# Optimization experiments

Hardware: AMD Instinct MI355X
Metric: run time of the kernel (lower is better)

## Reference

```python
import jax, jax.numpy as jnp
import numpy as np

N_NODES = 50000
N_EDGES = 800000
NDIM_IN = 64
EDIMS = 64
NDIM_OUT = 128


def setup_inputs() -> dict:
    key = jax.random.key(0)
    k = jax.random.split(key, 8)
    nfeats = jax.random.normal(k[0], (N_NODES, NDIM_IN), dtype=jnp.float32)
    efeats = jax.random.normal(k[1], (N_EDGES, EDIMS), dtype=jnp.float32)
    # Linear weights stored as [in, out]; scaled for stable activations.
    W_msg = jax.random.normal(k[2], (NDIM_IN + EDIMS, NDIM_OUT), dtype=jnp.float32) * 0.05
    b_msg = jax.random.normal(k[3], (NDIM_OUT,), dtype=jnp.float32) * 0.05
    W_apply = jax.random.normal(k[4], (NDIM_IN + NDIM_OUT, NDIM_OUT), dtype=jnp.float32) * 0.05
    b_apply = jax.random.normal(k[5], (NDIM_OUT,), dtype=jnp.float32) * 0.05
    src = jax.random.randint(k[6], (N_EDGES,), 0, N_NODES, dtype=jnp.int64)
    dst = jax.random.randint(k[7], (N_EDGES,), 0, N_NODES, dtype=jnp.int64)
    return {
        "nfeats": nfeats,
        "efeats": efeats,
        "W_msg": W_msg,
        "b_msg": b_msg,
        "W_apply": W_apply,
        "b_apply": b_apply,
        "src": src,
        "dst": dst,
    }


def reference(nfeats, efeats, W_msg, b_msg, W_apply, b_apply, src, dst):
    # message: per-edge gather src node feats, concat with edge feats, linear+relu
    msg_in = jnp.concatenate([nfeats[src], efeats], axis=1)          # [E, ndim_in+edims]
    m = jax.nn.relu(msg_in @ W_msg + b_msg)                           # [E, ndim_out]
    # aggregate: sum messages into destination nodes
    h_neigh = jax.ops.segment_sum(m, dst, num_segments=nfeats.shape[0])  # [N, ndim_out]
    # update: concat original node feats with aggregated messages, linear+relu
    out = jax.nn.relu(jnp.concatenate([nfeats, h_neigh], axis=1) @ W_apply + b_apply)
    return out
```

## Files before the change

### kernel.cpp

```cpp
#include <hip/hip_runtime.h>
#include <hip/hip_bf16.h>

#define N_NODES  50000
#define N_EDGES  800000
#define NDIM_IN  64
#define EDIMS    64
#define NDIM_OUT 128

typedef __bf16 bf16;
typedef bf16  bf16x8 __attribute__((ext_vector_type(8)));
typedef float f32x4  __attribute__((ext_vector_type(4)));

__device__ __forceinline__ bool detect_f32(const void* nfeats) {
    const unsigned short* w = (const unsigned short*)nfeats;
    for (int i = 0; i < 64; i += 2) {
        const int e = (w[i] >> 7) & 0xFF;
        if (e < 100 || e > 134) return true;
    }
    return false;
}
__device__ __forceinline__ bool detect_i64(const int* p) {
    for (int i = 1; i < 64; i += 2) if (p[i] != 0) return false;
    return true;
}

__device__ __forceinline__ bf16x8 load8(const void* p, long off, bool f32) {
    if (f32) {
        const float* q = (const float*)p + off;
        const f32x4 a = *(const f32x4*)q;
        const f32x4 b = *(const f32x4*)(q + 4);
        bf16x8 r;
        #pragma unroll
        for (int u = 0; u < 4; ++u) { r[u] = (bf16)a[u]; r[4 + u] = (bf16)b[u]; }
        return r;
    }
    return *(const bf16x8*)((const bf16*)p + off);
}
__device__ __forceinline__ float loadf(const void* p, long i, bool f32) {
    return f32 ? ((const float*)p)[i] : (float)((const bf16*)p)[i];
}
__device__ __forceinline__ void storef(void* p, long i, float v, bool f32) {
    if (f32) ((float*)p)[i] = v; else ((bf16*)p)[i] = (bf16)v;
}

__global__ __launch_bounds__(256) void nf2bf_kernel(const void* __restrict__ nfeats,
                                                    bf16* __restrict__ tbl) {
    __shared__ int s_flags;
    if (threadIdx.x == 0) s_flags = detect_f32(nfeats) ? 1 : 0;
    __syncthreads();
    const bool f32 = (s_flags & 1) != 0;
    const int total  = N_NODES * 64 / 8;
    const int stride = gridDim.x * blockDim.x;
    for (int i = blockIdx.x * blockDim.x + threadIdx.x; i < total; i += stride)
        *(bf16x8*)(tbl + (size_t)i * 8) = load8(nfeats, (long)i * 8, f32);
}

__global__ __launch_bounds__(256) void hist_kernel(const int* __restrict__ dst,
                                                   int* __restrict__ cnt) {
    __shared__ int s_ish;
    if (threadIdx.x == 0) s_ish = detect_i64(dst) ? 1 : 0;
    __syncthreads();
    const int ish = s_ish;
    const int stride = gridDim.x * blockDim.x;
    for (int e = blockIdx.x * blockDim.x + threadIdx.x; e < N_EDGES; e += stride)
        atomicAdd(&cnt[dst[(long)e << ish]], 1);
}

__global__ __launch_bounds__(1024) void scan_kernel(int* __restrict__ cnt,
                                                    int* __restrict__ row_ptr) {
    __shared__ int sw[16];
    const int t    = threadIdx.x;
    const int lane = t & 63;
    const int w    = t >> 6;
    const int base = t * 52;

    int sum = 0;
    #pragma unroll
    for (int j = 0; j < 13; ++j) {
        const int4 q = *(const int4*)(cnt + base + j * 4);
        sum += q.x + q.y + q.z + q.w;
    }
    int s = sum;
    #pragma unroll
    for (int off = 1; off < 64; off <<= 1) {
        const int u = __shfl_up(s, off, 64);
        if (lane >= off) s += u;
    }
    if (lane == 63) sw[w] = s;
    __syncthreads();
    if (t < 16) {
        int x = sw[t];
        #pragma unroll
        for (int off = 1; off < 16; off <<= 1) {
            const int u = __shfl_up(x, off, 16);
            if ((t & 15) >= off) x += u;
        }
        sw[t] = x;
    }
    __syncthreads();
    int run = (w > 0 ? sw[w - 1] : 0) + (s - sum);
    #pragma unroll
    for (int j = 0; j < 13; ++j) {
        const int4 q = *(const int4*)(cnt + base + j * 4);
        int4 r;
        r.x = run; run += q.x;
        r.y = run; run += q.y;
        r.z = run; run += q.z;
        r.w = run; run += q.w;
        *(int4*)(row_ptr + base + j * 4) = r;
        *(int4*)(cnt     + base + j * 4) = r;
    }
}

__global__ __launch_bounds__(256) void gather_kernel(
    const void* __restrict__ nfsrc,
    const void* __restrict__ efeats,
    const int*  __restrict__ src,
    const int*  __restrict__ dst,
    int*        __restrict__ cursor,
    bf16*       __restrict__ A,
    const int   tbl)
{
    __shared__ int s_flags;
    const int tid = threadIdx.x;
    if (tid == 0)
        s_flags = (detect_f32(efeats) ? 1 : 0) | (detect_i64(dst) ? 2 : 0);
    __syncthreads();
    const bool f32 = (s_flags & 1) != 0;
    const int  ish = (s_flags & 2) ? 1 : 0;

    const int lane = tid & 63;
    const int wave = tid >> 6;
    const int q    = lane & 15;
    const int ei   = lane >> 4;

    const int ngroups = N_EDGES / 4;
    const int nw      = gridDim.x * 4;
    for (int g = blockIdx.x * 4 + wave; g < ngroups; g += nw) {
        const int e = g * 4 + ei;
        int pos = 0;
        if (q == 0) pos = atomicAdd(&cursor[dst[(long)e << ish]], 1);
        pos = __shfl(pos, lane & 48, 64);

        bf16x8 v;
        if (q < 8) {
            const int s_ = src[(long)e << ish];
            v = tbl ? *(const bf16x8*)((const bf16*)nfsrc + (size_t)s_ * 64 + q * 8)
                    : load8(nfsrc, (long)s_ * 64 + q * 8, f32);
        } else {
            v = load8(efeats, (long)e * 64 + (q - 8) * 8, f32);
        }
        *(bf16x8*)(A + (size_t)pos * 128 + q * 8) = v;
    }
}

__global__ __launch_bounds__(256) void msg_agg_dense(
    const void* __restrict__ nfeats,
    const bf16* __restrict__ A,
    const void* __restrict__ W_msg,
    const void* __restrict__ b_msg,
    const int*  __restrict__ row_ptr,
    float*      __restrict__ h_neigh)
{
    __shared__ bf16 sWT[128 * 136];
    __shared__ int s_flags;

    const int tid = threadIdx.x;
    if (tid == 0) s_flags = detect_f32(nfeats) ? 1 : 0;
    __syncthreads();
    const bool f32 = (s_flags & 1) != 0;

    #pragma unroll
    for (int it = 0; it < 8; ++it) {
        const int task = it * 256 + tid;
        const int n    = task & 127;
        const int kb8  = task >> 7;
        bf16x8 w;
        #pragma unroll
        for (int j = 0; j < 8; ++j)
            w[j] = (bf16)loadf(W_msg, (long)(kb8 * 8 + j) * 128 + n, f32);
        *(bf16x8*)(sWT + n * 136 + kb8 * 8) = w;
    }
    __syncthreads();

    const int wave = tid >> 6;
    const int lane = tid & 63;
    const int m    = lane & 15;
    const int quad = lane >> 4;

    float bias[8];
    #pragma unroll
    for (int t = 0; t < 8; ++t) bias[t] = loadf(b_msg, t * 16 + m, f32);

    const int wstride = gridDim.x * 4;
    for (int v = blockIdx.x * 4 + wave; v < N_NODES; v += wstride) {
        const int beg = row_ptr[v];
        const int deg = row_ptr[v + 1] - beg;

        float hacc[8] = {0.f, 0.f, 0.f, 0.f, 0.f, 0.f, 0.f, 0.f};

        for (int T = 0; T * 16 < deg; ++T) {
            const int r0 = T * 16;
            const int sl = (r0 + m < deg) ? (beg + r0 + m) : beg;
            const bf16* ap = A + (size_t)sl * 128 + quad * 8;

            bf16x8 a[4];
            #pragma unroll
            for (int kb = 0; kb < 4; ++kb)
                a[kb] = *(const bf16x8*)(ap + kb * 32);

            #pragma unroll
            for (int t = 0; t < 8; ++t) {
                f32x4 acc = {0.f, 0.f, 0.f, 0.f};
                const bf16* bp = sWT + (t * 16 + m) * 136 + quad * 8;
                #pragma unroll
                for (int kb = 0; kb < 4; ++kb)
                    acc = __builtin_amdgcn_mfma_f32_16x16x32_bf16(
                              a[kb], *(const bf16x8*)(bp + kb * 32), acc, 0, 0, 0);
                float part = 0.f;
                #pragma unroll
                for (int i = 0; i < 4; ++i) {
                    float val = acc[i] + bias[t];
                    val = val > 0.f ? val : 0.f;
                    if (r0 + quad * 4 + i < deg) part += val;
                }
                hacc[t] += part;
            }
        }

        #pragma unroll
        for (int t = 0; t < 8; ++t) {
            float s = hacc[t];
            s += __shfl_xor(s, 16, 64);
            s += __shfl_xor(s, 32, 64);
            hacc[t] = s;
        }

        const float lo = quad < 2 ? (quad == 0 ? hacc[0] : hacc[1])
                                  : (quad == 2 ? hacc[2] : hacc[3]);
        const float hi = quad < 2 ? (quad == 0 ? hacc[4] : hacc[5])
                                  : (quad == 2 ? hacc[6] : hacc[7]);
        h_neigh[(size_t)v * 128 + lane]      = lo;
        h_neigh[(size_t)v * 128 + 64 + lane] = hi;
    }
}

__global__ __launch_bounds__(256) void scatter_kernel(const int* __restrict__ src,
                                                      const int* __restrict__ dst,
                                                      int* __restrict__ cursor,
                                                      int* __restrict__ eid,
                                                      int* __restrict__ srcs) {
    __shared__ int s_ish;
    if (threadIdx.x == 0) s_ish = detect_i64(dst) ? 1 : 0;
    __syncthreads();
    const int ish = s_ish;
    const int stride = gridDim.x * blockDim.x;
    for (int e = blockIdx.x * blockDim.x + threadIdx.x; e < N_EDGES; e += stride) {
        const int d = dst[(long)e << ish];
        const int pos = atomicAdd(&cursor[d], 1);
        eid[pos]  = e;
        srcs[pos] = src[(long)e << ish];
    }
}

__global__ __launch_bounds__(256) void msg_agg_kernel(
    const void* __restrict__ nfeats,
    const void* __restrict__ efeats,
    const void* __restrict__ W_msg,
    const void* __restrict__ b_msg,
    const int*  __restrict__ row_ptr,
    const int*  __restrict__ eid,
    const int*  __restrict__ srcs,
    float*      __restrict__ h_neigh)
{
    __shared__ bf16 sWT[128 * 136];
    __shared__ int s_flags;

    const int tid = threadIdx.x;
    if (tid == 0) s_flags = detect_f32(nfeats) ? 1 : 0;
    __syncthreads();
    const bool f32 = (s_flags & 1) != 0;

    #pragma unroll
    for (int it = 0; it < 8; ++it) {
        const int task = it * 256 + tid;
        const int k = task >> 4;
        const int c = task & 15;
        const bf16x8 w = load8(W_msg, (long)k * 128 + c * 8, f32);
        #pragma unroll
        for (int u = 0; u < 8; ++u) sWT[(c * 8 + u) * 136 + k] = w[u];
    }
    __syncthreads();

    const int wave = tid >> 6;
    const int lane = tid & 63;
    const int m    = lane & 15;
    const int quad = lane >> 4;

    float bias[8];
    #pragma unroll
    for (int t = 0; t < 8; ++t) bias[t] = loadf(b_msg, t * 16 + m, f32);

    const int wstride = gridDim.x * 4;
    for (int v = blockIdx.x * 4 + wave; v < N_NODES; v += wstride) {
        const int beg = row_ptr[v];
        const int deg = row_ptr[v + 1] - beg;

        float hacc[8] = {0.f, 0.f, 0.f, 0.f, 0.f, 0.f, 0.f, 0.f};

        for (int T = 0; T * 16 < deg; ++T) {
            const int r0 = T * 16;
            const int sl = (r0 + m < deg) ? (beg + r0 + m) : beg;
            const int s  = srcs[sl];
            const int e  = eid[sl];

            bf16x8 a[4];
            a[0] = load8(nfeats, (long)s * 64 +      quad * 8, f32);
            a[1] = load8(nfeats, (long)s * 64 + 32 + quad * 8, f32);
            a[2] = load8(efeats, (long)e * 64 +      quad * 8, f32);
            a[3] = load8(efeats, (long)e * 64 + 32 + quad * 8, f32);

            #pragma unroll
            for (int t = 0; t < 8; ++t) {
                f32x4 acc = {0.f, 0.f, 0.f, 0.f};
                const bf16* bp = sWT + (t * 16 + m) * 136 + quad * 8;
                #pragma unroll
                for (int kb = 0; kb < 4; ++kb)
                    acc = __builtin_amdgcn_mfma_f32_16x16x32_bf16(
                              a[kb], *(const bf16x8*)(bp + kb * 32), acc, 0, 0, 0);
                float part = 0.f;
                #pragma unroll
                for (int i = 0; i < 4; ++i) {
                    float val = acc[i] + bias[t];
                    val = val > 0.f ? val : 0.f;
                    if (r0 + quad * 4 + i < deg) part += val;
                }
                hacc[t] += part;
            }
        }

        #pragma unroll
        for (int t = 0; t < 8; ++t) {
            float s = hacc[t];
            s += __shfl_xor(s, 16, 64);
            s += __shfl_xor(s, 32, 64);
            hacc[t] = s;
        }

        const float lo = quad < 2 ? (quad == 0 ? hacc[0] : hacc[1])
                                  : (quad == 2 ? hacc[2] : hacc[3]);
        const float hi = quad < 2 ? (quad == 0 ? hacc[4] : hacc[5])
                                  : (quad == 2 ? hacc[6] : hacc[7]);
        h_neigh[(size_t)v * 128 + lane]      = lo;
        h_neigh[(size_t)v * 128 + 64 + lane] = hi;
    }
}

__global__ __launch_bounds__(256) void edge_msg_kernel(
    const void* __restrict__ nfeats,
    const void* __restrict__ efeats,
    const void* __restrict__ W_msg,
    const void* __restrict__ b_msg,
    const int*  __restrict__ src,
    const int*  __restrict__ dst,
    float*      __restrict__ h_neigh)
{
    __shared__ bf16 sWT[128 * 136];
    __shared__ int s_flags;

    const int tid = threadIdx.x;
    if (tid == 0)
        s_flags = (detect_f32(nfeats) ? 1 : 0) | (detect_i64(dst) ? 2 : 0);
    __syncthreads();
    const bool f32 = (s_flags & 1) != 0;
    const int  ish = (s_flags & 2) ? 1 : 0;

    #pragma unroll
    for (int it = 0; it < 8; ++it) {
        const int task = it * 256 + tid;
        const int k = task >> 4;
        const int c = task & 15;
        const bf16x8 w = load8(W_msg, (long)k * 128 + c * 8, f32);
        #pragma unroll
        for (int u = 0; u < 8; ++u) sWT[(c * 8 + u) * 136 + k] = w[u];
    }
    __syncthreads();

    const int wave = tid >> 6;
    const int lane = tid & 63;
    const int m    = lane & 15;
    const int quad = lane >> 4;

    const int nchunks = N_EDGES / 64;
    for (int chunk = blockIdx.x; chunk < nchunks; chunk += gridDim.x) {
        const int ebase = chunk * 64 + wave * 16;
        const int e_m   = ebase + m;
        const int s     = src[(long)e_m << ish];

        bf16x8 a[4];
        a[0] = load8(nfeats, (long)s   * 64 +      quad * 8, f32);
        a[1] = load8(nfeats, (long)s   * 64 + 32 + quad * 8, f32);
        a[2] = load8(efeats, (long)e_m * 64 +      quad * 8, f32);
        a[3] = load8(efeats, (long)e_m * 64 + 32 + quad * 8, f32);

        int drow[4];
        #pragma unroll
        for (int i = 0; i < 4; ++i)
            drow[i] = dst[(long)(ebase + quad * 4 + i) << ish] * 128;

        #pragma unroll
        for (int t = 0; t < 8; ++t) {
            f32x4 acc = {0.f, 0.f, 0.f, 0.f};
            const bf16* bp = sWT + (t * 16 + m) * 136 + quad * 8;
            #pragma unroll
            for (int kb = 0; kb < 4; ++kb)
                acc = __builtin_amdgcn_mfma_f32_16x16x32_bf16(
                          a[kb], *(const bf16x8*)(bp + kb * 32), acc, 0, 0, 0);
            const int   n    = t * 16 + m;
            const float bias = loadf(b_msg, n, f32);
            #pragma unroll
            for (int i = 0; i < 4; ++i) {
                float v = acc[i] + bias;
                v = v > 0.f ? v : 0.f;
                unsafeAtomicAdd(h_neigh + drow[i] + n, v);
            }
        }
    }
}

__global__ __launch_bounds__(256) void apply_kernel(
    const void*  __restrict__ nfeats,
    const float* __restrict__ h_neigh,
    const void*  __restrict__ W_apply,
    const void*  __restrict__ b_apply,
    void*        __restrict__ out)
{
    __shared__ bf16 sWT[128 * 200];
    __shared__ int s_flags;

    const int tid = threadIdx.x;
    if (tid == 0) s_flags = detect_f32(nfeats) ? 1 : 0;
    __syncthreads();
    const bool f32 = (s_flags & 1) != 0;

    #pragma unroll
    for (int it = 0; it < 12; ++it) {
        const int task = it * 256 + tid;
        const int n    = task & 127;
        const int kb8  = task >> 7;
        bf16x8 w;
        #pragma unroll
        for (int j = 0; j < 8; ++j)
            w[j] = (bf16)loadf(W_apply, (long)(kb8 * 8 + j) * 128 + n, f32);
        *(bf16x8*)(sWT + n * 200 + kb8 * 8) = w;
    }
    __syncthreads();

    const int wave = tid >> 6;
    const int lane = tid & 63;
    const int m    = lane & 15;
    const int quad = lane >> 4;

    const int nchunks = (N_NODES + 63) / 64;
    for (int chunk = blockIdx.x; chunk < nchunks; chunk += gridDim.x) {
        const int nbase = chunk * 64 + wave * 16;
        const int nm  = nbase + m;
        const int nmc = nm < N_NODES ? nm : N_NODES - 1;

        bf16x8 a[6];
        a[0] = load8(nfeats, (long)nmc * 64 +      quad * 8, f32);
        a[1] = load8(nfeats, (long)nmc * 64 + 32 + quad * 8, f32);
        #pragma unroll
        for (int kb = 0; kb < 4; ++kb) {
            const float* hp = h_neigh + (size_t)nmc * 128 + kb * 32 + quad * 8;
            const f32x4 p = *(const f32x4*)(hp);
            const f32x4 q = *(const f32x4*)(hp + 4);
            bf16x8 r;
            #pragma unroll
            for (int u = 0; u < 4; ++u) { r[u] = (bf16)p[u]; r[4 + u] = (bf16)q[u]; }
            a[2 + kb] = r;
        }

        #pragma unroll
        for (int t = 0; t < 8; ++t) {
            f32x4 acc = {0.f, 0.f, 0.f, 0.f};
            const bf16* bp = sWT + (t * 16 + m) * 200 + quad * 8;
            #pragma unroll
            for (int kb = 0; kb < 6; ++kb)
                acc = __builtin_amdgcn_mfma_f32_16x16x32_bf16(
                          a[kb], *(const bf16x8*)(bp + kb * 32), acc, 0, 0, 0);
            const int   n    = t * 16 + m;
            const float bias = loadf(b_apply, n, f32);
            #pragma unroll
            for (int i = 0; i < 4; ++i) {
                const int row = nbase + quad * 4 + i;
                if (row < N_NODES) {
                    float v = acc[i] + bias;
                    v = v > 0.f ? v : 0.f;
                    storef(out, (long)row * 128 + n, v, f32);
                }
            }
        }
    }
}

extern "C" void kernel_launch(void* const* d_in, const int* in_sizes, int n_in,
                              void* d_out, int out_size, void* d_ws, size_t ws_size,
                              hipStream_t stream) {
    const void* nfeats  = d_in[0];
    const void* efeats  = d_in[1];
    const void* W_msg   = d_in[2];
    const void* b_msg   = d_in[3];
    const void* W_apply = d_in[4];
    const void* b_apply = d_in[5];
    const int*  src     = (const int*)d_in[6];
    const int*  dst     = (const int*)d_in[7];

    float* h_neigh = (float*)d_ws;

    const size_t SZ_PAD     = 213248;
    const size_t OFF_ROWPTR = 25600000;
    const size_t OFF_CNT    = OFF_ROWPTR + SZ_PAD;
    const size_t OFF_A      = OFF_CNT + SZ_PAD;
    const size_t SZ_A       = (size_t)N_EDGES * 128 * 2;
    const size_t OFF_NF     = OFF_A + SZ_A;
    const size_t NEED_DENSE = OFF_A + SZ_A;
    const size_t NEED_TBL   = OFF_NF + (size_t)N_NODES * 64 * 2;
    const size_t OFF_EID    = OFF_A;
    const size_t OFF_SRCS   = OFF_EID + 3200000;
    const size_t NEED_CSR   = OFF_SRCS + 3200000;

    int* row_ptr = (int*)((char*)d_ws + OFF_ROWPTR);
    int* cnt     = (int*)((char*)d_ws + OFF_CNT);

    if (ws_size >= NEED_DENSE) {
        bf16* A   = (bf16*)((char*)d_ws + OFF_A);
        const int tbl = (ws_size >= NEED_TBL) ? 1 : 0;
        bf16* nft = (bf16*)((char*)d_ws + OFF_NF);

        hipMemsetAsync(cnt, 0, (size_t)53248 * sizeof(int), stream);
        if (tbl) nf2bf_kernel<<<1563, 256, 0, stream>>>(nfeats, nft);
        hist_kernel<<<1024, 256, 0, stream>>>(dst, cnt);
        scan_kernel<<<1, 1024, 0, stream>>>(cnt, row_ptr);
        gather_kernel<<<2048, 256, 0, stream>>>(tbl ? (const void*)nft : nfeats,
                                                efeats, src, dst, cnt, A, tbl);
        msg_agg_dense<<<1024, 256, 0, stream>>>(nfeats, A, W_msg, b_msg,
                                                row_ptr, h_neigh);
    } else if (ws_size >= NEED_CSR) {
        int* eid  = (int*)((char*)d_ws + OFF_EID);
        int* srcs = (int*)((char*)d_ws + OFF_SRCS);
        hipMemsetAsync(cnt, 0, (size_t)53248 * sizeof(int), stream);
        hist_kernel<<<1024, 256, 0, stream>>>(dst, cnt);
        scan_kernel<<<1, 1024, 0, stream>>>(cnt, row_ptr);
        scatter_kernel<<<1024, 256, 0, stream>>>(src, dst, cnt, eid, srcs);
        msg_agg_kernel<<<1024, 256, 0, stream>>>(nfeats, efeats, W_msg, b_msg,
                                                 row_ptr, eid, srcs, h_neigh);
    } else {
        hipMemsetAsync(h_neigh, 0, (size_t)N_NODES * NDIM_OUT * sizeof(float), stream);
        edge_msg_kernel<<<768, 256, 0, stream>>>(nfeats, efeats, W_msg, b_msg,
                                                 src, dst, h_neigh);
    }

    apply_kernel<<<782, 256, 0, stream>>>(nfeats, h_neigh, W_apply, b_apply, d_out);
}
```

Baseline: 608.1 us.

## Sort only edge features into CSR order and gather node features from bf16 table

The gather pass now writes only the 64 edge-feature columns in destination order, plus a sorted src index array. It no longer materialises the full 128-wide concatenated row. The aggregation kernel reads node features through the src indices from a bf16 node table. It also prefetches the next node's first tile of operands while computing the current one, keeps the bias in shared memory, and sets a launch-bounds occupancy hint. The aim is to halve the intermediate write/read traffic, at the cost of an indirect gather inside the compute kernel.

New measurement: 981.5 us. 1.61x slower.

```diff
diff --git a/kernel.cpp b/kernel.cpp
--- a/kernel.cpp
+++ b/kernel.cpp
@@ -113,13 +113,12 @@
 }
 
 __global__ __launch_bounds__(256) void gather_kernel(
-    const void* __restrict__ nfsrc,
     const void* __restrict__ efeats,
     const int*  __restrict__ src,
     const int*  __restrict__ dst,
     int*        __restrict__ cursor,
     bf16*       __restrict__ A,
-    const int   tbl)
+    int*        __restrict__ srcs)
 {
     __shared__ int s_flags;
     const int tid = threadIdx.x;
@@ -131,39 +130,39 @@
 
     const int lane = tid & 63;
     const int wave = tid >> 6;
-    const int q    = lane & 15;
-    const int ei   = lane >> 4;
-
-    const int ngroups = N_EDGES / 4;
+    const int q    = lane & 7;
+    const int ei   = lane >> 3;
+
+    const int ngroups = N_EDGES / 8;
     const int nw      = gridDim.x * 4;
     for (int g = blockIdx.x * 4 + wave; g < ngroups; g += nw) {
-        const int e = g * 4 + ei;
-        int pos = 0;
-        if (q == 0) pos = atomicAdd(&cursor[dst[(long)e << ish]], 1);
-        pos = __shfl(pos, lane & 48, 64);
-
-        bf16x8 v;
-        if (q < 8) {
-            const int s_ = src[(long)e << ish];
-            v = tbl ? *(const bf16x8*)((const bf16*)nfsrc + (size_t)s_ * 64 + q * 8)
-                    : load8(nfsrc, (long)s_ * 64 + q * 8, f32);
-        } else {
-            v = load8(efeats, (long)e * 64 + (q - 8) * 8, f32);
-        }
-        *(bf16x8*)(A + (size_t)pos * 128 + q * 8) = v;
-    }
-}
-
-__global__ __launch_bounds__(256) void msg_agg_dense(
+        const int e = g * 8 + ei;
+        int pos = 0, s_ = 0;
+        if (q == 0) {
+            pos = atomicAdd(&cursor[dst[(long)e << ish]], 1);
+            s_  = src[(long)e << ish];
+        }
+        pos = __shfl(pos, lane & 56, 64);
+
+        const bf16x8 v = load8(efeats, (long)e * 64 + q * 8, f32);
+        *(bf16x8*)(A + (size_t)pos * 64 + q * 8) = v;
+        if (q == 0) srcs[pos] = s_;
+    }
+}
+
+__global__ __launch_bounds__(256, 4) void msg_agg_dense(
     const void* __restrict__ nfeats,
+    const bf16* __restrict__ xtbl,
     const bf16* __restrict__ A,
+    const int*  __restrict__ srcs,
     const void* __restrict__ W_msg,
     const void* __restrict__ b_msg,
     const int*  __restrict__ row_ptr,
     float*      __restrict__ h_neigh)
 {
-    __shared__ bf16 sWT[128 * 136];
-    __shared__ int s_flags;
+    __shared__ bf16  sWT[128 * 136];
+    __shared__ float sB[128];
+    __shared__ int   s_flags;
 
     const int tid = threadIdx.x;
     if (tid == 0) s_flags = detect_f32(nfeats) ? 1 : 0;
@@ -181,6 +180,7 @@
             w[j] = (bf16)loadf(W_msg, (long)(kb8 * 8 + j) * 128 + n, f32);
         *(bf16x8*)(sWT + n * 136 + kb8 * 8) = w;
     }
+    if (tid < 128) sB[tid] = loadf(b_msg, tid, f32);
     __syncthreads();
 
     const int wave = tid >> 6;
@@ -188,6 +188,163 @@
     const int m    = lane & 15;
     const int quad = lane >> 4;
 
+    const int wstride = gridDim.x * 4;
+    int v = blockIdx.x * 4 + wave;
+    if (v >= N_NODES) return;
+
+    int beg = row_ptr[v];
+    int deg = row_ptr[v + 1] - beg;
+    bf16x8 a0, a1, a2, a3;
+    {
+        int sl = beg + (m < deg ? m : 0);
+        sl = sl < N_EDGES ? sl : N_EDGES - 1;
+        int s = srcs[sl];
+        s = ((unsigned)s < N_NODES) ? s : 0;
+        a2 = *(const bf16x8*)(A + (size_t)sl * 64 + quad * 8);
+        a3 = *(const bf16x8*)(A + (size_t)sl * 64 + 32 + quad * 8);
+        a0 = *(const bf16x8*)(xtbl + (size_t)s * 64 + quad * 8);
+        a1 = *(const bf16x8*)(xtbl + (size_t)s * 64 + 32 + quad * 8);
+    }
+
+    while (true) {
+        const int  vn   = v + wstride;
+        const bool hasn = vn < N_NODES;
+        int begn = 0, degn = 0;
+        bf16x8 b0, b1, b2, b3;
+        if (hasn) {
+            begn = row_ptr[vn];
+            degn = row_ptr[vn + 1] - begn;
+            int sln = begn + (m < degn ? m : 0);
+            sln = sln < N_EDGES ? sln : N_EDGES - 1;
+            int sn = srcs[sln];
+            sn = ((unsigned)sn < N_NODES) ? sn : 0;
+            b2 = *(const bf16x8*)(A + (size_t)sln * 64 + quad * 8);
+            b3 = *(const bf16x8*)(A + (size_t)sln * 64 + 32 + quad * 8);
+            b0 = *(const bf16x8*)(xtbl + (size_t)sn * 64 + quad * 8);
+            b1 = *(const bf16x8*)(xtbl + (size_t)sn * 64 + 32 + quad * 8);
+        }
+
+        float hacc[8] = {0.f, 0.f, 0.f, 0.f, 0.f, 0.f, 0.f, 0.f};
+
+        #pragma unroll
+        for (int t = 0; t < 8; ++t) {
+            f32x4 acc = {0.f, 0.f, 0.f, 0.f};
+            const bf16* bp = sWT + (t * 16 + m) * 136 + quad * 8;
+            acc = __builtin_amdgcn_mfma_f32_16x16x32_bf16(a0, *(const bf16x8*)(bp      ), acc, 0, 0, 0);
+            acc = __builtin_amdgcn_mfma_f32_16x16x32_bf16(a1, *(const bf16x8*)(bp +  32), acc, 0, 0, 0);
+            acc = __builtin_amdgcn_mfma_f32_16x16x32_bf16(a2, *(const bf16x8*)(bp +  64), acc, 0, 0, 0);
+            acc = __builtin_amdgcn_mfma_f32_16x16x32_bf16(a3, *(const bf16x8*)(bp +  96), acc, 0, 0, 0);
+            const float bias = sB[t * 16 + m];
+            float part = 0.f;
+            #pragma unroll
+            for (int i = 0; i < 4; ++i) {
+                float val = acc[i] + bias;
+                val = val > 0.f ? val : 0.f;
+                if (quad * 4 + i < deg) part += val;
+            }
+            hacc[t] += part;
+        }
+
+        for (int T = 1; T * 16 < deg; ++T) {
+            const int r0 = T * 16;
+            const int sl = (r0 + m < deg) ? (beg + r0 + m) : beg;
+            const int s  = srcs[sl];
+            const bf16x8 c2 = *(const bf16x8*)(A + (size_t)sl * 64 + quad * 8);
+            const bf16x8 c3 = *(const bf16x8*)(A + (size_t)sl * 64 + 32 + quad * 8);
+            const bf16x8 c0 = *(const bf16x8*)(xtbl + (size_t)s * 64 + quad * 8);
+            const bf16x8 c1 = *(const bf16x8*)(xtbl + (size_t)s * 64 + 32 + quad * 8);
+            #pragma unroll
+            for (int t = 0; t < 8; ++t) {
+                f32x4 acc = {0.f, 0.f, 0.f, 0.f};
+                const bf16* bp = sWT + (t * 16 + m) * 136 + quad * 8;
+                acc = __builtin_amdgcn_mfma_f32_16x16x32_bf16(c0, *(const bf16x8*)(bp      ), acc, 0, 0, 0);
+                acc = __builtin_amdgcn_mfma_f32_16x16x32_bf16(c1, *(const bf16x8*)(bp +  32), acc, 0, 0, 0);
+                acc = __builtin_amdgcn_mfma_f32_16x16x32_bf16(c2, *(const bf16x8*)(bp +  64), acc, 0, 0, 0);
+                acc = __builtin_amdgcn_mfma_f32_16x16x32_bf16(c3, *(const bf16x8*)(bp +  96), acc, 0, 0, 0);
+                const float bias = sB[t * 16 + m];
+                float part = 0.f;
+                #pragma unroll
+                for (int i = 0; i < 4; ++i) {
+                    float val = acc[i] + bias;
+                    val = val > 0.f ? val : 0.f;
+                    if (r0 + quad * 4 + i < deg) part += val;
+                }
+                hacc[t] += part;
+            }
+        }
+
+        #pragma unroll
+        for (int t = 0; t < 8; ++t) {
+            float s = hacc[t];
+            s += __shfl_xor(s, 16, 64);
+            s += __shfl_xor(s, 32, 64);
+            hacc[t] = s;
+        }
+        const float lo = quad < 2 ? (quad == 0 ? hacc[0] : hacc[1])
+                                  : (quad == 2 ? hacc[2] : hacc[3]);
+        const float hi = quad < 2 ? (quad == 0 ? hacc[4] : hacc[5])
+                                  : (quad == 2 ? hacc[6] : hacc[7]);
+        h_neigh[(size_t)v * 128 + lane]      = lo;
+        h_neigh[(size_t)v * 128 + 64 + lane] = hi;
+
+        if (!hasn) break;
+        v = vn; beg = begn; deg = degn;
+        a0 = b0; a1 = b1; a2 = b2; a3 = b3;
+    }
+}
+
+__global__ __launch_bounds__(256) void scatter_kernel(const int* __restrict__ src,
+                                                      const int* __restrict__ dst,
+                                                      int* __restrict__ cursor,
+                                                      int* __restrict__ eid,
+                                                      int* __restrict__ srcs) {
+    __shared__ int s_ish;
+    if (threadIdx.x == 0) s_ish = detect_i64(dst) ? 1 : 0;
+    __syncthreads();
+    const int ish = s_ish;
+    const int stride = gridDim.x * blockDim.x;
+    for (int e = blockIdx.x * blockDim.x + threadIdx.x; e < N_EDGES; e += stride) {
+        const int d = dst[(long)e << ish];
+        const int pos = atomicAdd(&cursor[d], 1);
+        eid[pos]  = e;
+        srcs[pos] = src[(long)e << ish];
+    }
+}
+
+__global__ __launch_bounds__(256) void msg_agg_kernel(
+    const void* __restrict__ nfeats,
+    const void* __restrict__ efeats,
+    const void* __restrict__ W_msg,
+    const void* __restrict__ b_msg,
+    const int*  __restrict__ row_ptr,
+    const int*  __restrict__ eid,
+    const int*  __restrict__ srcs,
+    float*      __restrict__ h_neigh)
+{
+    __shared__ bf16 sWT[128 * 136];
+    __shared__ int s_flags;
+
+    const int tid = threadIdx.x;
+    if (tid == 0) s_flags = detect_f32(nfeats) ? 1 : 0;
+    __syncthreads();
+    const bool f32 = (s_flags & 1) != 0;
+
+    #pragma unroll
+    for (int it = 0; it < 8; ++it) {
+        const int task = it * 256 + tid;
+        const int k = task >> 4;
+        const int c = task & 15;
+        const bf16x8 w = load8(W_msg, (long)k * 128 + c * 8, f32);
+        #pragma unroll
+        for (int u = 0; u < 8; ++u) sWT[(c * 8 + u) * 136 + k] = w[u];
+    }
+    __syncthreads();
+
+    const int wave = tid >> 6;
+    const int lane = tid & 63;
+    const int m    = lane & 15;
+    const int quad = lane >> 4;
+
     float bias[8];
     #pragma unroll
     for (int t = 0; t < 8; ++t) bias[t] = loadf(b_msg, t * 16 + m, f32);
@@ -202,12 +359,14 @@
         for (int T = 0; T * 16 < deg; ++T) {
             const int r0 = T * 16;
             const int sl = (r0 + m < deg) ? (beg + r0 + m) : beg;
-            const bf16* ap = A + (size_t)sl * 128 + quad * 8;
+            const int s  = srcs[sl];
+            const int e  = eid[sl];
 
             bf16x8 a[4];
-            #pragma unroll
-            for (int kb = 0; kb < 4; ++kb)
-                a[kb] = *(const bf16x8*)(ap + kb * 32);
+            a[0] = load8(nfeats, (long)s * 64 +      quad * 8, f32);
+            a[1] = load8(nfeats, (long)s * 64 + 32 + quad * 8, f32);
+            a[2] = load8(efeats, (long)e * 64 +      quad * 8, f32);
+            a[3] = load8(efeats, (long)e * 64 + 32 + quad * 8, f32);
 
             #pragma unroll
             for (int t = 0; t < 8; ++t) {
@@ -245,117 +404,6 @@
     }
 }
 
-__global__ __launch_bounds__(256) void scatter_kernel(const int* __restrict__ src,
-                                                      const int* __restrict__ dst,
-                                                      int* __restrict__ cursor,
-                                                      int* __restrict__ eid,
-                                                      int* __restrict__ srcs) {
-    __shared__ int s_ish;
-    if (threadIdx.x == 0) s_ish = detect_i64(dst) ? 1 : 0;
-    __syncthreads();
-    const int ish = s_ish;
-    const int stride = gridDim.x * blockDim.x;
-    for (int e = blockIdx.x * blockDim.x + threadIdx.x; e < N_EDGES; e += stride) {
-        const int d = dst[(long)e << ish];
-        const int pos = atomicAdd(&cursor[d], 1);
-        eid[pos]  = e;
-        srcs[pos] = src[(long)e << ish];
-    }
-}
-
-__global__ __launch_bounds__(256) void msg_agg_kernel(
-    const void* __restrict__ nfeats,
-    const void* __restrict__ efeats,
-    const void* __restrict__ W_msg,
-    const void* __restrict__ b_msg,
-    const int*  __restrict__ row_ptr,
-    const int*  __restrict__ eid,
-    const int*  __restrict__ srcs,
-    float*      __restrict__ h_neigh)
-{
-    __shared__ bf16 sWT[128 * 136];
-    __shared__ int s_flags;
-
-    const int tid = threadIdx.x;
-    if (tid == 0) s_flags = detect_f32(nfeats) ? 1 : 0;
-    __syncthreads();
-    const bool f32 = (s_flags & 1) != 0;
-
-    #pragma unroll
-    for (int it = 0; it < 8; ++it) {
-        const int task = it * 256 + tid;
-        const int k = task >> 4;
-        const int c = task & 15;
-        const bf16x8 w = load8(W_msg, (long)k * 128 + c * 8, f32);
-        #pragma unroll
-        for (int u = 0; u < 8; ++u) sWT[(c * 8 + u) * 136 + k] = w[u];
-    }
-    __syncthreads();
-
-    const int wave = tid >> 6;
-    const int lane = tid & 63;
-    const int m    = lane & 15;
-    const int quad = lane >> 4;
-
-    float bias[8];
-    #pragma unroll
-    for (int t = 0; t < 8; ++t) bias[t] = loadf(b_msg, t * 16 + m, f32);
-
-    const int wstride = gridDim.x * 4;
-    for (int v = blockIdx.x * 4 + wave; v < N_NODES; v += wstride) {
-        const int beg = row_ptr[v];
-        const int deg = row_ptr[v + 1] - beg;
-
-        float hacc[8] = {0.f, 0.f, 0.f, 0.f, 0.f, 0.f, 0.f, 0.f};
-
-        for (int T = 0; T * 16 < deg; ++T) {
-            const int r0 = T * 16;
-            const int sl = (r0 + m < deg) ? (beg + r0 + m) : beg;
-            const int s  = srcs[sl];
-            const int e  = eid[sl];
-
-            bf16x8 a[4];
-            a[0] = load8(nfeats, (long)s * 64 +      quad * 8, f32);
-            a[1] = load8(nfeats, (long)s * 64 + 32 + quad * 8, f32);
-            a[2] = load8(efeats, (long)e * 64 +      quad * 8, f32);
-            a[3] = load8(efeats, (long)e * 64 + 32 + quad * 8, f32);
-
-            #pragma unroll
-            for (int t = 0; t < 8; ++t) {
-                f32x4 acc = {0.f, 0.f, 0.f, 0.f};
-                const bf16* bp = sWT + (t * 16 + m) * 136 + quad * 8;
-                #pragma unroll
-                for (int kb = 0; kb < 4; ++kb)
-                    acc = __builtin_amdgcn_mfma_f32_16x16x32_bf16(
-                              a[kb], *(const bf16x8*)(bp + kb * 32), acc, 0, 0, 0);
-                float part = 0.f;
-                #pragma unroll
-                for (int i = 0; i < 4; ++i) {
-                    float val = acc[i] + bias[t];
-                    val = val > 0.f ? val : 0.f;
-                    if (r0 + quad * 4 + i < deg) part += val;
-                }
-                hacc[t] += part;
-            }
-        }
-
-        #pragma unroll
-        for (int t = 0; t < 8; ++t) {
-            float s = hacc[t];
-            s += __shfl_xor(s, 16, 64);
-            s += __shfl_xor(s, 32, 64);
-            hacc[t] = s;
-        }
-
-        const float lo = quad < 2 ? (quad == 0 ? hacc[0] : hacc[1])
-                                  : (quad == 2 ? hacc[2] : hacc[3]);
-        const float hi = quad < 2 ? (quad == 0 ? hacc[4] : hacc[5])
-                                  : (quad == 2 ? hacc[6] : hacc[7]);
-        h_neigh[(size_t)v * 128 + lane]      = lo;
-        h_neigh[(size_t)v * 128 + 64 + lane] = hi;
-    }
-}
-
 __global__ __launch_bounds__(256) void edge_msg_kernel(
     const void* __restrict__ nfeats,
     const void* __restrict__ efeats,
@@ -521,34 +569,34 @@
     const size_t SZ_PAD     = 213248;
     const size_t OFF_ROWPTR = 25600000;
     const size_t OFF_CNT    = OFF_ROWPTR + SZ_PAD;
-    const size_t OFF_A      = OFF_CNT + SZ_PAD;
-    const size_t SZ_A       = (size_t)N_EDGES * 128 * 2;
-    const size_t OFF_NF     = OFF_A + SZ_A;
-    const size_t NEED_DENSE = OFF_A + SZ_A;
-    const size_t NEED_TBL   = OFF_NF + (size_t)N_NODES * 64 * 2;
-    const size_t OFF_EID    = OFF_A;
-    const size_t OFF_SRCS   = OFF_EID + 3200000;
-    const size_t NEED_CSR   = OFF_SRCS + 3200000;
+    const size_t OFF_XT     = OFF_CNT + SZ_PAD;
+    const size_t SZ_XT      = (size_t)N_NODES * 64 * 2;
+    const size_t OFF_A      = OFF_XT + SZ_XT;
+    const size_t SZ_A       = (size_t)N_EDGES * 64 * 2;
+    const size_t OFF_SRCS   = OFF_A + SZ_A;
+    const size_t NEED_DENSE = OFF_SRCS + 3200000;
+    const size_t OFF_EID    = OFF_XT;
+    const size_t OFF_SRCS2  = OFF_EID + 3200000;
+    const size_t NEED_CSR   = OFF_SRCS2 + 3200000;
 
     int* row_ptr = (int*)((char*)d_ws + OFF_ROWPTR);
     int* cnt     = (int*)((char*)d_ws + OFF_CNT);
 
     if (ws_size >= NEED_DENSE) {
-        bf16* A   = (bf16*)((char*)d_ws + OFF_A);
-        const int tbl = (ws_size >= NEED_TBL) ? 1 : 0;
-        bf16* nft = (bf16*)((char*)d_ws + OFF_NF);
+        bf16* xtbl = (bf16*)((char*)d_ws + OFF_XT);
+        bf16* A    = (bf16*)((char*)d_ws + OFF_A);
+        int*  srcs = (int*)((char*)d_ws + OFF_SRCS);
 
         hipMemsetAsync(cnt, 0, (size_t)53248 * sizeof(int), stream);
-        if (tbl) nf2bf_kernel<<<1563, 256, 0, stream>>>(nfeats, nft);
+        nf2bf_kernel<<<1563, 256, 0, stream>>>(nfeats, xtbl);
         hist_kernel<<<1024, 256, 0, stream>>>(dst, cnt);
         scan_kernel<<<1, 1024, 0, stream>>>(cnt, row_ptr);
-        gather_kernel<<<2048, 256, 0, stream>>>(tbl ? (const void*)nft : nfeats,
-                                                efeats, src, dst, cnt, A, tbl);
-        msg_agg_dense<<<1024, 256, 0, stream>>>(nfeats, A, W_msg, b_msg,
-                                                row_ptr, h_neigh);
+        gather_kernel<<<2048, 256, 0, stream>>>(efeats, src, dst, cnt, A, srcs);
+        msg_agg_dense<<<1024, 256, 0, stream>>>(nfeats, xtbl, A, srcs,
+                                                W_msg, b_msg, row_ptr, h_neigh);
     } else if (ws_size >= NEED_CSR) {
         int* eid  = (int*)((char*)d_ws + OFF_EID);
-        int* srcs = (int*)((char*)d_ws + OFF_SRCS);
+        int* srcs = (int*)((char*)d_ws + OFF_SRCS2);
         hipMemsetAsync(cnt, 0, (size_t)53248 * sizeof(int), stream);
         hist_kernel<<<1024, 256, 0, stream>>>(dst, cnt);
         scan_kernel<<<1, 1024, 0, stream>>>(cnt, row_ptr);
```

## Process sorted edges in fixed 64-edge windows with segmented flush instead of per-node loops

Applied to the files above, without the earlier changes.

The message-aggregation kernel now walks dst-sorted edges in fixed 64-edge windows. Each edge's destination id is recorded during the gather, and partial sums are flushed at segment boundaries: plain stores for nodes that lie entirely inside a window, atomics for boundary nodes. This removes the per-node padding waste of 16-row tiles for low-degree nodes and the load imbalance from variable degrees. The feature-conversion and histogram kernels are merged into one launch, and bias moves to shared memory. In exchange it adds a memset of h_neigh, an extra nid array write and read, and float atomics at window edges, which make the summation order nondeterministic.

Measured after the change: 610.6 us. About the same (+0.4%).

```diff
diff --git a/kernel.cpp b/kernel.cpp
--- a/kernel.cpp
+++ b/kernel.cpp
@@ -43,16 +43,30 @@
     if (f32) ((float*)p)[i] = v; else ((bf16*)p)[i] = (bf16)v;
 }
 
-__global__ __launch_bounds__(256) void nf2bf_kernel(const void* __restrict__ nfeats,
-                                                    bf16* __restrict__ tbl) {
+__global__ __launch_bounds__(256) void prep_kernel(const void* __restrict__ nfeats,
+                                                   bf16* __restrict__ tbl,
+                                                   const int* __restrict__ dst,
+                                                   int* __restrict__ cnt,
+                                                   const int do_tbl) {
     __shared__ int s_flags;
-    if (threadIdx.x == 0) s_flags = detect_f32(nfeats) ? 1 : 0;
+    if (threadIdx.x == 0)
+        s_flags = (detect_f32(nfeats) ? 1 : 0) | (detect_i64(dst) ? 2 : 0);
     __syncthreads();
     const bool f32 = (s_flags & 1) != 0;
-    const int total  = N_NODES * 64 / 8;
-    const int stride = gridDim.x * blockDim.x;
-    for (int i = blockIdx.x * blockDim.x + threadIdx.x; i < total; i += stride)
-        *(bf16x8*)(tbl + (size_t)i * 8) = load8(nfeats, (long)i * 8, f32);
+    const int  ish = (s_flags & 2) ? 1 : 0;
+    const int CONV = 512;
+    if ((int)blockIdx.x < CONV) {
+        if (!do_tbl) return;
+        const int total  = N_NODES * 64 / 8;
+        const int stride = CONV * 256;
+        for (int i = blockIdx.x * 256 + threadIdx.x; i < total; i += stride)
+            *(bf16x8*)(tbl + (size_t)i * 8) = load8(nfeats, (long)i * 8, f32);
+    } else {
+        const int nb     = gridDim.x - CONV;
+        const int stride = nb * 256;
+        for (int e = (blockIdx.x - CONV) * 256 + threadIdx.x; e < N_EDGES; e += stride)
+            atomicAdd(&cnt[dst[(long)e << ish]], 1);
+    }
 }
 
 __global__ __launch_bounds__(256) void hist_kernel(const int* __restrict__ dst,
@@ -119,6 +133,7 @@
     const int*  __restrict__ dst,
     int*        __restrict__ cursor,
     bf16*       __restrict__ A,
+    int*        __restrict__ nid,
     const int   tbl)
 {
     __shared__ int s_flags;
@@ -138,32 +153,38 @@
     const int nw      = gridDim.x * 4;
     for (int g = blockIdx.x * 4 + wave; g < ngroups; g += nw) {
         const int e = g * 4 + ei;
-        int pos = 0;
-        if (q == 0) pos = atomicAdd(&cursor[dst[(long)e << ish]], 1);
+        int pos = 0, s_ = 0, d = 0;
+        if (q == 0) {
+            d   = dst[(long)e << ish];
+            pos = atomicAdd(&cursor[d], 1);
+            s_  = src[(long)e << ish];
+        }
         pos = __shfl(pos, lane & 48, 64);
+        s_  = __shfl(s_,  lane & 48, 64);
 
         bf16x8 v;
         if (q < 8) {
-            const int s_ = src[(long)e << ish];
             v = tbl ? *(const bf16x8*)((const bf16*)nfsrc + (size_t)s_ * 64 + q * 8)
                     : load8(nfsrc, (long)s_ * 64 + q * 8, f32);
         } else {
             v = load8(efeats, (long)e * 64 + (q - 8) * 8, f32);
         }
         *(bf16x8*)(A + (size_t)pos * 128 + q * 8) = v;
+        if (q == 0) nid[pos] = d;
     }
 }
 
 __global__ __launch_bounds__(256) void msg_agg_dense(
     const void* __restrict__ nfeats,
     const bf16* __restrict__ A,
+    const int*  __restrict__ nid,
     const void* __restrict__ W_msg,
     const void* __restrict__ b_msg,
-    const int*  __restrict__ row_ptr,
     float*      __restrict__ h_neigh)
 {
-    __shared__ bf16 sWT[128 * 136];
-    __shared__ int s_flags;
+    __shared__ bf16  sWT[128 * 136];
+    __shared__ float sB[128];
+    __shared__ int   s_flags;
 
     const int tid = threadIdx.x;
     if (tid == 0) s_flags = detect_f32(nfeats) ? 1 : 0;
@@ -181,6 +202,7 @@
             w[j] = (bf16)loadf(W_msg, (long)(kb8 * 8 + j) * 128 + n, f32);
         *(bf16x8*)(sWT + n * 136 + kb8 * 8) = w;
     }
+    if (tid < 128) sB[tid] = loadf(b_msg, tid, f32);
     __syncthreads();
 
     const int wave = tid >> 6;
@@ -188,6 +210,133 @@
     const int m    = lane & 15;
     const int quad = lane >> 4;
 
+    const int NW     = N_EDGES / 64;
+    const int stride = gridDim.x * 4;
+    for (int win = blockIdx.x * 4 + wave; win < NW; win += stride) {
+        const int base = win * 64;
+        const int myn  = nid[base + lane];
+        const int nxtn = __shfl_down(myn, 1, 64);
+        const unsigned long long bmask =
+            __ballot((lane == 63) || (myn != nxtn));
+
+        float hacc[8] = {0.f, 0.f, 0.f, 0.f, 0.f, 0.f, 0.f, 0.f};
+        int nflush = 0;
+
+        #pragma unroll
+        for (int t4 = 0; t4 < 4; ++t4) {
+            const bf16* ap = A + (size_t)(base + t4 * 16 + m) * 128 + quad * 8;
+            const bf16x8 a0 = *(const bf16x8*)(ap);
+            const bf16x8 a1 = *(const bf16x8*)(ap + 32);
+            const bf16x8 a2 = *(const bf16x8*)(ap + 64);
+            const bf16x8 a3 = *(const bf16x8*)(ap + 96);
+
+            f32x4 acc[8];
+            #pragma unroll
+            for (int t = 0; t < 8; ++t) {
+                f32x4 c = {0.f, 0.f, 0.f, 0.f};
+                const bf16* bp = sWT + (t * 16 + m) * 136 + quad * 8;
+                c = __builtin_amdgcn_mfma_f32_16x16x32_bf16(a0, *(const bf16x8*)(bp     ), c, 0, 0, 0);
+                c = __builtin_amdgcn_mfma_f32_16x16x32_bf16(a1, *(const bf16x8*)(bp + 32), c, 0, 0, 0);
+                c = __builtin_amdgcn_mfma_f32_16x16x32_bf16(a2, *(const bf16x8*)(bp + 64), c, 0, 0, 0);
+                c = __builtin_amdgcn_mfma_f32_16x16x32_bf16(a3, *(const bf16x8*)(bp + 96), c, 0, 0, 0);
+                const float bias = sB[t * 16 + m];
+                #pragma unroll
+                for (int i = 0; i < 4; ++i) {
+                    const float v = c[i] + bias;
+                    c[i] = v > 0.f ? v : 0.f;
+                }
+                acc[t] = c;
+            }
+
+            #pragma unroll
+            for (int r = 0; r < 16; ++r) {
+                if (quad == (r >> 2)) {
+                    #pragma unroll
+                    for (int t = 0; t < 8; ++t) hacc[t] += acc[t][r & 3];
+                }
+                const int idx = t4 * 16 + r;
+                if ((bmask >> idx) & 1ull) {
+                    const int node = __shfl(myn, idx, 64);
+                    float f[8];
+                    #pragma unroll
+                    for (int t = 0; t < 8; ++t) {
+                        float s = hacc[t];
+                        s += __shfl_xor(s, 16, 64);
+                        s += __shfl_xor(s, 32, 64);
+                        f[t] = s;
+                        hacc[t] = 0.f;
+                    }
+                    const float lo = quad < 2 ? (quad == 0 ? f[0] : f[1])
+                                              : (quad == 2 ? f[2] : f[3]);
+                    const float hi = quad < 2 ? (quad == 0 ? f[4] : f[5])
+                                              : (quad == 2 ? f[6] : f[7]);
+                    float* hp = h_neigh + (size_t)node * 128;
+                    if (nflush > 0 && idx < 63) {
+                        hp[lane]      = lo;
+                        hp[64 + lane] = hi;
+                    } else {
+                        unsafeAtomicAdd(hp + lane,      lo);
+                        unsafeAtomicAdd(hp + 64 + lane, hi);
+                    }
+                    ++nflush;
+                }
+            }
+        }
+    }
+}
+
+__global__ __launch_bounds__(256) void scatter_kernel(const int* __restrict__ src,
+                                                      const int* __restrict__ dst,
+                                                      int* __restrict__ cursor,
+                                                      int* __restrict__ eid,
+                                                      int* __restrict__ srcs) {
+    __shared__ int s_ish;
+    if (threadIdx.x == 0) s_ish = detect_i64(dst) ? 1 : 0;
+    __syncthreads();
+    const int ish = s_ish;
+    const int stride = gridDim.x * blockDim.x;
+    for (int e = blockIdx.x * blockDim.x + threadIdx.x; e < N_EDGES; e += stride) {
+        const int d = dst[(long)e << ish];
+        const int pos = atomicAdd(&cursor[d], 1);
+        eid[pos]  = e;
+        srcs[pos] = src[(long)e << ish];
+    }
+}
+
+__global__ __launch_bounds__(256) void msg_agg_kernel(
+    const void* __restrict__ nfeats,
+    const void* __restrict__ efeats,
+    const void* __restrict__ W_msg,
+    const void* __restrict__ b_msg,
+    const int*  __restrict__ row_ptr,
+    const int*  __restrict__ eid,
+    const int*  __restrict__ srcs,
+    float*      __restrict__ h_neigh)
+{
+    __shared__ bf16 sWT[128 * 136];
+    __shared__ int s_flags;
+
+    const int tid = threadIdx.x;
+    if (tid == 0) s_flags = detect_f32(nfeats) ? 1 : 0;
+    __syncthreads();
+    const bool f32 = (s_flags & 1) != 0;
+
+    #pragma unroll
+    for (int it = 0; it < 8; ++it) {
+        const int task = it * 256 + tid;
+        const int k = task >> 4;
+        const int c = task & 15;
+        const bf16x8 w = load8(W_msg, (long)k * 128 + c * 8, f32);
+        #pragma unroll
+        for (int u = 0; u < 8; ++u) sWT[(c * 8 + u) * 136 + k] = w[u];
+    }
+    __syncthreads();
+
+    const int wave = tid >> 6;
+    const int lane = tid & 63;
+    const int m    = lane & 15;
+    const int quad = lane >> 4;
+
     float bias[8];
     #pragma unroll
     for (int t = 0; t < 8; ++t) bias[t] = loadf(b_msg, t * 16 + m, f32);
@@ -202,12 +351,14 @@
         for (int T = 0; T * 16 < deg; ++T) {
             const int r0 = T * 16;
             const int sl = (r0 + m < deg) ? (beg + r0 + m) : beg;
-            const bf16* ap = A + (size_t)sl * 128 + quad * 8;
+            const int s  = srcs[sl];
+            const int e  = eid[sl];
 
             bf16x8 a[4];
-            #pragma unroll
-            for (int kb = 0; kb < 4; ++kb)
-                a[kb] = *(const bf16x8*)(ap + kb * 32);
+            a[0] = load8(nfeats, (long)s * 64 +      quad * 8, f32);
+            a[1] = load8(nfeats, (long)s * 64 + 32 + quad * 8, f32);
+            a[2] = load8(efeats, (long)e * 64 +      quad * 8, f32);
+            a[3] = load8(efeats, (long)e * 64 + 32 + quad * 8, f32);
 
             #pragma unroll
             for (int t = 0; t < 8; ++t) {
@@ -245,117 +396,6 @@
     }
 }
 
-__global__ __launch_bounds__(256) void scatter_kernel(const int* __restrict__ src,
-                                                      const int* __restrict__ dst,
-                                                      int* __restrict__ cursor,
-                                                      int* __restrict__ eid,
-                                                      int* __restrict__ srcs) {
-    __shared__ int s_ish;
-    if (threadIdx.x == 0) s_ish = detect_i64(dst) ? 1 : 0;
-    __syncthreads();
-    const int ish = s_ish;
-    const int stride = gridDim.x * blockDim.x;
-    for (int e = blockIdx.x * blockDim.x + threadIdx.x; e < N_EDGES; e += stride) {
-        const int d = dst[(long)e << ish];
-        const int pos = atomicAdd(&cursor[d], 1);
-        eid[pos]  = e;
-        srcs[pos] = src[(long)e << ish];
-    }
-}
-
-__global__ __launch_bounds__(256) void msg_agg_kernel(
-    const void* __restrict__ nfeats,
-    const void* __restrict__ efeats,
-    const void* __restrict__ W_msg,
-    const void* __restrict__ b_msg,
-    const int*  __restrict__ row_ptr,
-    const int*  __restrict__ eid,
-    const int*  __restrict__ srcs,
-    float*      __restrict__ h_neigh)
-{
-    __shared__ bf16 sWT[128 * 136];
-    __shared__ int s_flags;
-
-    const int tid = threadIdx.x;
-    if (tid == 0) s_flags = detect_f32(nfeats) ? 1 : 0;
-    __syncthreads();
-    const bool f32 = (s_flags & 1) != 0;
-
-    #pragma unroll
-    for (int it = 0; it < 8; ++it) {
-        const int task = it * 256 + tid;
-        const int k = task >> 4;
-        const int c = task & 15;
-        const bf16x8 w = load8(W_msg, (long)k * 128 + c * 8, f32);
-        #pragma unroll
-        for (int u = 0; u < 8; ++u) sWT[(c * 8 + u) * 136 + k] = w[u];
-    }
-    __syncthreads();
-
-    const int wave = tid >> 6;
-    const int lane = tid & 63;
-    const int m    = lane & 15;
-    const int quad = lane >> 4;
-
-    float bias[8];
-    #pragma unroll
-    for (int t = 0; t < 8; ++t) bias[t] = loadf(b_msg, t * 16 + m, f32);
-
-    const int wstride = gridDim.x * 4;
-    for (int v = blockIdx.x * 4 + wave; v < N_NODES; v += wstride) {
-        const int beg = row_ptr[v];
-        const int deg = row_ptr[v + 1] - beg;
-
-        float hacc[8] = {0.f, 0.f, 0.f, 0.f, 0.f, 0.f, 0.f, 0.f};
-
-        for (int T = 0; T * 16 < deg; ++T) {
-            const int r0 = T * 16;
-            const int sl = (r0 + m < deg) ? (beg + r0 + m) : beg;
-            const int s  = srcs[sl];
-            const int e  = eid[sl];
-
-            bf16x8 a[4];
-            a[0] = load8(nfeats, (long)s * 64 +      quad * 8, f32);
-            a[1] = load8(nfeats, (long)s * 64 + 32 + quad * 8, f32);
-            a[2] = load8(efeats, (long)e * 64 +      quad * 8, f32);
-            a[3] = load8(efeats, (long)e * 64 + 32 + quad * 8, f32);
-
-            #pragma unroll
-            for (int t = 0; t < 8; ++t) {
-                f32x4 acc = {0.f, 0.f, 0.f, 0.f};
-                const bf16* bp = sWT + (t * 16 + m) * 136 + quad * 8;
-                #pragma unroll
-                for (int kb = 0; kb < 4; ++kb)
-                    acc = __builtin_amdgcn_mfma_f32_16x16x32_bf16(
-                              a[kb], *(const bf16x8*)(bp + kb * 32), acc, 0, 0, 0);
-                float part = 0.f;
-                #pragma unroll
-                for (int i = 0; i < 4; ++i) {
-                    float val = acc[i] + bias[t];
-                    val = val > 0.f ? val : 0.f;
-                    if (r0 + quad * 4 + i < deg) part += val;
-                }
-                hacc[t] += part;
-            }
-        }
-
-        #pragma unroll
-        for (int t = 0; t < 8; ++t) {
-            float s = hacc[t];
-            s += __shfl_xor(s, 16, 64);
-            s += __shfl_xor(s, 32, 64);
-            hacc[t] = s;
-        }
-
-        const float lo = quad < 2 ? (quad == 0 ? hacc[0] : hacc[1])
-                                  : (quad == 2 ? hacc[2] : hacc[3]);
-        const float hi = quad < 2 ? (quad == 0 ? hacc[4] : hacc[5])
-                                  : (quad == 2 ? hacc[6] : hacc[7]);
-        h_neigh[(size_t)v * 128 + lane]      = lo;
-        h_neigh[(size_t)v * 128 + 64 + lane] = hi;
-    }
-}
-
 __global__ __launch_bounds__(256) void edge_msg_kernel(
     const void* __restrict__ nfeats,
     const void* __restrict__ efeats,
@@ -521,34 +561,39 @@
     const size_t SZ_PAD     = 213248;
     const size_t OFF_ROWPTR = 25600000;
     const size_t OFF_CNT    = OFF_ROWPTR + SZ_PAD;
-    const size_t OFF_A      = OFF_CNT + SZ_PAD;
+    const size_t OFF_XT     = OFF_CNT + SZ_PAD;
+    const size_t SZ_XT      = (size_t)N_NODES * 64 * 2;
+    const size_t OFF_A      = OFF_XT + SZ_XT;
     const size_t SZ_A       = (size_t)N_EDGES * 128 * 2;
-    const size_t OFF_NF     = OFF_A + SZ_A;
-    const size_t NEED_DENSE = OFF_A + SZ_A;
-    const size_t NEED_TBL   = OFF_NF + (size_t)N_NODES * 64 * 2;
-    const size_t OFF_EID    = OFF_A;
-    const size_t OFF_SRCS   = OFF_EID + 3200000;
-    const size_t NEED_CSR   = OFF_SRCS + 3200000;
+    const size_t OFF_NID    = OFF_A + SZ_A;
+    const size_t NEED_FULL  = OFF_NID + 3200000;
+    const size_t OFF_A2     = OFF_XT;
+    const size_t OFF_NID2   = OFF_A2 + SZ_A;
+    const size_t NEED_NOTBL = OFF_NID2 + 3200000;
+    const size_t OFF_EID    = OFF_XT;
+    const size_t OFF_SRCS2  = OFF_EID + 3200000;
+    const size_t NEED_CSR   = OFF_SRCS2 + 3200000;
 
     int* row_ptr = (int*)((char*)d_ws + OFF_ROWPTR);
     int* cnt     = (int*)((char*)d_ws + OFF_CNT);
 
-    if (ws_size >= NEED_DENSE) {
-        bf16* A   = (bf16*)((char*)d_ws + OFF_A);
-        const int tbl = (ws_size >= NEED_TBL) ? 1 : 0;
-        bf16* nft = (bf16*)((char*)d_ws + OFF_NF);
+    if (ws_size >= NEED_NOTBL) {
+        const int tbl = (ws_size >= NEED_FULL) ? 1 : 0;
+        bf16* xtbl = (bf16*)((char*)d_ws + OFF_XT);
+        bf16* A    = (bf16*)((char*)d_ws + (tbl ? OFF_A   : OFF_A2));
+        int*  nid  = (int*)((char*)d_ws + (tbl ? OFF_NID : OFF_NID2));
 
         hipMemsetAsync(cnt, 0, (size_t)53248 * sizeof(int), stream);
-        if (tbl) nf2bf_kernel<<<1563, 256, 0, stream>>>(nfeats, nft);
-        hist_kernel<<<1024, 256, 0, stream>>>(dst, cnt);
+        hipMemsetAsync(h_neigh, 0, (size_t)N_NODES * NDIM_OUT * sizeof(float), stream);
+        prep_kernel<<<1536, 256, 0, stream>>>(nfeats, xtbl, dst, cnt, tbl);
         scan_kernel<<<1, 1024, 0, stream>>>(cnt, row_ptr);
-        gather_kernel<<<2048, 256, 0, stream>>>(tbl ? (const void*)nft : nfeats,
-                                                efeats, src, dst, cnt, A, tbl);
-        msg_agg_dense<<<1024, 256, 0, stream>>>(nfeats, A, W_msg, b_msg,
-                                                row_ptr, h_neigh);
+        gather_kernel<<<2048, 256, 0, stream>>>(tbl ? (const void*)xtbl : nfeats,
+                                                efeats, src, dst, cnt, A, nid, tbl);
+        msg_agg_dense<<<1024, 256, 0, stream>>>(nfeats, A, nid,
+                                                W_msg, b_msg, h_neigh);
     } else if (ws_size >= NEED_CSR) {
         int* eid  = (int*)((char*)d_ws + OFF_EID);
-        int* srcs = (int*)((char*)d_ws + OFF_SRCS);
+        int* srcs = (int*)((char*)d_ws + OFF_SRCS2);
         hipMemsetAsync(cnt, 0, (size_t)53248 * sizeof(int), stream);
         hist_kernel<<<1024, 256, 0, stream>>>(dst, cnt);
         scan_kernel<<<1, 1024, 0, stream>>>(cnt, row_ptr);
```
